# Performance work log

Measured on AMD Instinct MI355X. Metric: run time of the kernel, lower is better.

## Reference

```python
import jax, jax.numpy as jnp
import numpy as np

B, L, S, E = 16, 2048, 2048, 512

def setup_inputs() -> dict:
    key = jax.random.key(0)
    k1, k2, k3 = jax.random.split(key, 3)
    queries = jax.random.normal(k1, (B, L, E), dtype=jnp.float32)
    keys = jax.random.normal(k2, (B, S, E), dtype=jnp.float32)
    values = jax.random.normal(k3, (B, S, E), dtype=jnp.float32)
    # default causal mask: True above the diagonal (positions to mask out)
    attn_mask = jnp.triu(jnp.ones((L, S), dtype=bool), k=1)
    return {"queries": queries, "keys": keys, "values": values, "attn_mask": attn_mask}

def reference(queries, keys, values, attn_mask):
    # queries [B,L,E], keys/values [B,S,E], attn_mask [L,S] bool (True = mask)
    scale = 1.0 / jnp.sqrt(jnp.asarray(queries.shape[-1], queries.dtype))
    scores = jnp.einsum('ble,bse->bls', queries, keys)  # [B,L,S]
    scores = jnp.where(attn_mask, -jnp.inf, scores) * scale
    attn = jax.nn.softmax(scores, axis=-1)  # dropout p=0.0 -> identity
    context = jnp.einsum('bls,bse->ble', attn, values)  # [B,L,E]
    return context
```

## Files before the change

### kernel.cpp

```cpp
#include <hip/hip_runtime.h>

typedef __attribute__((ext_vector_type(4))) float f32x4;
typedef __attribute__((ext_vector_type(16))) float f32x16;
typedef __attribute__((ext_vector_type(8))) short s16x8;
typedef __attribute__((ext_vector_type(8))) unsigned short u16x8;
typedef __attribute__((ext_vector_type(4))) unsigned short u16x4;

#define NB 16
#define SEQ 2048
#define DIM 512
#define QB 64
#define KB 256

__device__ __forceinline__ unsigned short f2bf(float x) {
  unsigned u = __float_as_uint(x);
  u += 0x7fffu + ((u >> 16) & 1u);
  return (unsigned short)(u >> 16);
}

__global__ __launch_bounds__(256) void kf_cvt_kernel(const float* __restrict__ in,
                                                     unsigned short* __restrict__ out) {
  __shared__ float ld[32 * 513];
  const float cs = 0.0637587224f;
  int blk = blockIdx.x;
  int b = blk >> 6, kv32 = blk & 63;
  int t = threadIdx.x;
  const float* src = in + ((size_t)b * SEQ + kv32 * 32) * DIM;
#pragma unroll
  for (int i = 0; i < 16; ++i) {
    int flat = (i * 256 + t) * 4;
    f32x4 a = *(const f32x4*)(src + flat);
    int row = flat >> 9, e = flat & 511;
    float* d = ld + row * 513 + e;
    d[0] = a[0]; d[1] = a[1]; d[2] = a[2]; d[3] = a[3];
  }
  __syncthreads();
  unsigned short* dst = out + (size_t)blk * 16384;
#pragma unroll
  for (int i = 0; i < 8; ++i) {
    int idx8 = i * 256 + t;
    int kstep = idx8 >> 6, ln = idx8 & 63;
    int row = ln & 31, hi = ln >> 5;
    const float* s = ld + row * 513 + kstep * 16 + hi * 8;
    u16x8 o;
#pragma unroll
    for (int j = 0; j < 8; ++j) o[j] = f2bf(s[j] * cs);
    *(u16x8*)(dst + (size_t)idx8 * 8) = o;
  }
}

__global__ __launch_bounds__(256) void vf_cvt_kernel(const float* __restrict__ in,
                                                     unsigned short* __restrict__ out) {
  __shared__ float ld[256 * 33];
  int blk = blockIdx.x;
  int kvc = blk & 7, e32 = (blk >> 3) & 15, b = blk >> 7;
  int t = threadIdx.x;
  const float* src = in + ((size_t)b * SEQ + kvc * 256) * DIM + e32 * 32;
  int r0 = t >> 2, part = t & 3;
#pragma unroll
  for (int i = 0; i < 4; ++i) {
    int row = i * 64 + r0;
    const float* s = src + (size_t)row * DIM + part * 8;
    f32x4 a0 = *(const f32x4*)s;
    f32x4 a1 = *(const f32x4*)(s + 4);
    float* d = ld + row * 33 + part * 8;
    d[0] = a0[0]; d[1] = a0[1]; d[2] = a0[2]; d[3] = a0[3];
    d[4] = a1[0]; d[5] = a1[1]; d[6] = a1[2]; d[7] = a1[3];
  }
  __syncthreads();
  unsigned short* dst = out + (size_t)blk * 8192;
#pragma unroll
  for (int i = 0; i < 4; ++i) {
    int idx8 = i * 256 + t;
    int ksl = idx8 >> 6, ln = idx8 & 63;
    int e = ln & 31, hi = ln >> 5;
    const float* s0 = ld + (ksl * 16 + hi * 8) * 33 + e;
    u16x8 o;
#pragma unroll
    for (int j = 0; j < 8; ++j) o[j] = f2bf(s0[j * 33]);
    *(u16x8*)(dst + (size_t)idx8 * 8) = o;
  }
}

__global__ __launch_bounds__(1024, 1) void attn_kernel(const float* __restrict__ qg,
                                                       const unsigned short* __restrict__ kf,
                                                       const unsigned short* __restrict__ vf,
                                                       float* __restrict__ out) {
  int b = blockIdx.x;
  int y = blockIdx.y;
  int qt = (y < 16) ? y : 47 - y;
  int q0 = qt * QB;

  int tid = threadIdx.x;
  int lane = tid & 63;
  int wid = tid >> 6;
  int l31 = lane & 31;
  int lhi = lane >> 5;
  int mg = wid >> 3, kvq = wid & 7;

  __shared__ unsigned short Qs[2][32][512];
  __shared__ unsigned short Pl[2][64][256];
  __shared__ float cmx[8][68];
  __shared__ float Fs[64];
  __shared__ float Ls[64];

  {
    int q = tid >> 4;
    int ec = (tid & 15) * 32;
    const float* src = qg + ((size_t)b * SEQ + q0 + q) * DIM + ec;
    float v[32];
#pragma unroll
    for (int i = 0; i < 8; ++i) {
      f32x4 a = *(const f32x4*)(src + i * 4);
      v[i * 4 + 0] = a[0]; v[i * 4 + 1] = a[1]; v[i * 4 + 2] = a[2]; v[i * 4 + 3] = a[3];
    }
    int mgq = q >> 5, lq = q & 31;
#pragma unroll
    for (int s = 0; s < 2; ++s) {
      int ks = (ec >> 4) + s;
#pragma unroll
      for (int h = 0; h < 2; ++h) {
        u16x8 o;
#pragma unroll
        for (int j = 0; j < 8; ++j) o[j] = f2bf(v[s * 16 + h * 8 + j]);
        *(u16x8*)&Qs[mgq][ks][(lq + 32 * h) * 8] = o;
      }
    }
  }
  __syncthreads();

  f32x16 oacc[2];
#pragma unroll
  for (int n = 0; n < 2; ++n)
#pragma unroll
    for (int r = 0; r < 16; ++r) oacc[n][r] = 0.f;

  float m_r = -1e30f, l_r = 0.f;
  int qi = mg * 32 + l31;
  unsigned swz = ((unsigned)(qi & 31)) << 4;

  const unsigned short* kfb = kf + ((size_t)b * 64) * 16384;
  int nt = (qt + 4) >> 2;

  for (int t = 0; t < nt; ++t) {
    int pb = t & 1;

    f32x16 sp;
#pragma unroll
    for (int r = 0; r < 16; ++r) sp[r] = 0.f;
    {
      const unsigned short* kp = kfb + ((size_t)(t * 8 + kvq) * 32) * 512 + lane * 8;
#pragma unroll 4
      for (int ks = 0; ks < 32; ++ks) {
        s16x8 a0 = *(const s16x8*)(kp + ks * 512);
        s16x8 b0 = *(const s16x8*)&Qs[mg][ks][lane * 8];
        sp = __builtin_amdgcn_mfma_f32_32x32x16_bf16(a0, b0, sp, 0, 0, 0);
      }
    }

    if (t == nt - 1) {
      int qgl = q0 + qi;
      int kvb = t * 256 + kvq * 32 + 4 * lhi;
#pragma unroll
      for (int r = 0; r < 16; ++r) {
        int kv = kvb + (r & 3) + 8 * (r >> 2);
        if (kv > qgl) sp[r] = -1e30f;
      }
    }

    float cm = sp[0];
#pragma unroll
    for (int r = 1; r < 16; ++r) cm = fmaxf(cm, sp[r]);
    cm = fmaxf(cm, __shfl_xor(cm, 32));
    if (lhi == 0) cmx[kvq][qi] = cm;
    __syncthreads();

    float mt = cmx[0][qi];
#pragma unroll
    for (int c = 1; c < 8; ++c) mt = fmaxf(mt, cmx[c][qi]);
    float m_new = fmaxf(m_r, mt);
    float fsc = exp2f(m_r - m_new);
    m_r = m_new;
    float ps = 0.f;
    u16x4 pk[4];
#pragma unroll
    for (int r = 0; r < 16; ++r) {
      float p = exp2f(sp[r] - m_new);
      ps += p;
      pk[r >> 2][r & 3] = f2bf(p);
    }
    l_r = l_r * fsc + ps;
    {
      char* prow = (char*)&Pl[pb][qi][0];
#pragma unroll
      for (int g = 0; g < 4; ++g) {
        unsigned kvbyte = (unsigned)(kvq * 64 + g * 16 + lhi * 8);
        *(u16x4*)(prow + (kvbyte ^ swz)) = pk[g];
      }
    }
    if (kvq == 0 && lhi == 0) Fs[qi] = fsc;
    __syncthreads();

    {
      f32x4 fr[2][4];
#pragma unroll
      for (int m2 = 0; m2 < 2; ++m2)
#pragma unroll
        for (int g = 0; g < 4; ++g)
          fr[m2][g] = *(const f32x4*)&Fs[m2 * 32 + g * 8 + lhi * 4];
#pragma unroll
      for (int m2 = 0; m2 < 2; ++m2)
#pragma unroll
        for (int r = 0; r < 16; ++r) oacc[m2][r] *= fr[m2][r >> 2][r & 3];

      const unsigned short* vpb =
          vf + (((size_t)b * 16 + wid) * 128 + t * 16) * 512 + lane * 8;
      const char* pr0 = (const char*)&Pl[pb][l31][0];
      const char* pr1 = (const char*)&Pl[pb][32 + l31][0];
      unsigned swzr = ((unsigned)l31) << 4;
#pragma unroll 4
      for (int ks = 0; ks < 16; ++ks) {
        unsigned kb0 = (unsigned)(ks * 32 + lhi * 16);
        s16x8 A0 = *(const s16x8*)(pr0 + (kb0 ^ swzr));
        s16x8 A1 = *(const s16x8*)(pr1 + (kb0 ^ swzr));
        s16x8 B0 = *(const s16x8*)(vpb + ks * 512);
        oacc[0] = __builtin_amdgcn_mfma_f32_32x32x16_bf16(A0, B0, oacc[0], 0, 0, 0);
        oacc[1] = __builtin_amdgcn_mfma_f32_32x32x16_bf16(A1, B0, oacc[1], 0, 0, 0);
      }
    }
  }

  {
    float* lsx = (float*)&Qs[0][0][0];
    __syncthreads();
    lsx[(kvq * 2 + lhi) * 68 + qi] = l_r;
    __syncthreads();
    if (tid < 64) {
      float s = 0.f;
#pragma unroll
      for (int c = 0; c < 16; ++c) s += lsx[c * 68 + tid];
      Ls[tid] = 1.f / s;
    }
    __syncthreads();
  }

  {
    f32x4 li[2][4];
#pragma unroll
    for (int m2 = 0; m2 < 2; ++m2)
#pragma unroll
      for (int g = 0; g < 4; ++g)
        li[m2][g] = *(const f32x4*)&Ls[m2 * 32 + g * 8 + lhi * 4];
#pragma unroll
    for (int m2 = 0; m2 < 2; ++m2)
#pragma unroll
      for (int r = 0; r < 16; ++r) {
        int row = m2 * 32 + (r & 3) + 8 * (r >> 2) + 4 * lhi;
        out[((size_t)b * SEQ + q0 + row) * DIM + wid * 32 + l31] =
            oacc[m2][r] * li[m2][r >> 2][r & 3];
      }
  }
}

extern "C" void kernel_launch(void* const* d_in, const int* in_sizes, int n_in,
                              void* d_out, int out_size, void* d_ws, size_t ws_size,
                              hipStream_t stream) {
  (void)in_sizes; (void)n_in; (void)out_size;
  const float* q = (const float*)d_in[0];
  const float* k = (const float*)d_in[1];
  const float* v = (const float*)d_in[2];
  float* out = (float*)d_out;
  const size_t nelem = (size_t)NB * SEQ * DIM;
  if (ws_size < 2 * nelem * sizeof(unsigned short)) return;
  unsigned short* kfw = (unsigned short*)d_ws;
  unsigned short* vfw = kfw + nelem;

  kf_cvt_kernel<<<NB * 64, 256, 0, stream>>>(k, kfw);
  vf_cvt_kernel<<<NB * 16 * 8, 256, 0, stream>>>(v, vfw);
  dim3 ag(NB, SEQ / QB);
  attn_kernel<<<ag, 1024, 0, stream>>>(q, kfw, vfw, out);
}
```

Measured before the change: 158.4 us.

## Software-pipeline PV of tile t-2 with QK of tile t, one barrier per iteration

Restructures the attention main loop so the P·V MFMAs for tile t-2 are interleaved with the Q·K^T MFMAs for tile t, and the two pending tiles are drained after the loop. The row-max scratch and rescale factors are double-buffered, which removes one __syncthreads per tile and gives the matrix cores two independent accumulation chains to overlap with global loads. The cost is higher register pressure from holding both accumulators and more operand loads inside one loop body. It also adds a separate epilogue code path for the last two tiles.

```diff
diff --git a/kernel.cpp b/kernel.cpp
--- a/kernel.cpp
+++ b/kernel.cpp
@@ -82,6 +82,37 @@
   }
 }
 
+__device__ __forceinline__ void pv_tile_fn(int u, f32x16* oacc,
+                                           const unsigned short* vfb,
+                                           const unsigned short (*Pl)[64][256],
+                                           const float (*Fs)[64], int lane) {
+  int l31 = lane & 31, lhi = lane >> 5;
+  int pb2 = u & 1;
+  const float* fsb = Fs[pb2];
+  f32x4 fr[2][4];
+#pragma unroll
+  for (int m2 = 0; m2 < 2; ++m2)
+#pragma unroll
+    for (int g = 0; g < 4; ++g) fr[m2][g] = *(const f32x4*)&fsb[m2 * 32 + g * 8 + lhi * 4];
+#pragma unroll
+  for (int m2 = 0; m2 < 2; ++m2)
+#pragma unroll
+    for (int r = 0; r < 16; ++r) oacc[m2][r] *= fr[m2][r >> 2][r & 3];
+  const unsigned short* vp = vfb + (size_t)u * 16 * 512 + lane * 8;
+  const char* pr0 = (const char*)&Pl[pb2][l31][0];
+  const char* pr1 = (const char*)&Pl[pb2][32 + l31][0];
+  unsigned swzr = ((unsigned)l31) << 4;
+#pragma unroll 4
+  for (int ks = 0; ks < 16; ++ks) {
+    unsigned kb0 = (unsigned)(ks * 32 + lhi * 16);
+    s16x8 A0 = *(const s16x8*)(pr0 + (kb0 ^ swzr));
+    s16x8 A1 = *(const s16x8*)(pr1 + (kb0 ^ swzr));
+    s16x8 B0 = *(const s16x8*)(vp + ks * 512);
+    oacc[0] = __builtin_amdgcn_mfma_f32_32x32x16_bf16(A0, B0, oacc[0], 0, 0, 0);
+    oacc[1] = __builtin_amdgcn_mfma_f32_32x32x16_bf16(A1, B0, oacc[1], 0, 0, 0);
+  }
+}
+
 __global__ __launch_bounds__(1024, 1) void attn_kernel(const float* __restrict__ qg,
                                                        const unsigned short* __restrict__ kf,
                                                        const unsigned short* __restrict__ vf,
@@ -100,8 +131,8 @@
 
   __shared__ unsigned short Qs[2][32][512];
   __shared__ unsigned short Pl[2][64][256];
-  __shared__ float cmx[8][68];
-  __shared__ float Fs[64];
+  __shared__ float cmx[2][8][68];
+  __shared__ float Fs[2][64];
   __shared__ float Ls[64];
 
   {
@@ -137,20 +168,54 @@
 
   float m_r = -1e30f, l_r = 0.f;
   int qi = mg * 32 + l31;
-  unsigned swz = ((unsigned)(qi & 31)) << 4;
+  unsigned swz = ((unsigned)l31) << 4;
 
   const unsigned short* kfb = kf + ((size_t)b * 64) * 16384;
+  const unsigned short* vfb = vf + ((size_t)b * 16 + wid) * 128 * 512;
   int nt = (qt + 4) >> 2;
 
   for (int t = 0; t < nt; ++t) {
-    int pb = t & 1;
-
     f32x16 sp;
 #pragma unroll
     for (int r = 0; r < 16; ++r) sp[r] = 0.f;
-    {
-      const unsigned short* kp = kfb + ((size_t)(t * 8 + kvq) * 32) * 512 + lane * 8;
+    const unsigned short* kp = kfb + ((size_t)(t * 8 + kvq) * 32) * 512 + lane * 8;
+
+    if (t >= 2) {
+      int u = t - 2, pb2 = u & 1;
+      {
+        const float* fsb = Fs[pb2];
+        f32x4 fr[2][4];
+#pragma unroll
+        for (int m2 = 0; m2 < 2; ++m2)
+#pragma unroll
+          for (int g = 0; g < 4; ++g)
+            fr[m2][g] = *(const f32x4*)&fsb[m2 * 32 + g * 8 + lhi * 4];
+#pragma unroll
+        for (int m2 = 0; m2 < 2; ++m2)
+#pragma unroll
+          for (int r = 0; r < 16; ++r) oacc[m2][r] *= fr[m2][r >> 2][r & 3];
+      }
+      const unsigned short* vp = vfb + (size_t)u * 16 * 512 + lane * 8;
+      const char* pr0 = (const char*)&Pl[pb2][l31][0];
+      const char* pr1 = (const char*)&Pl[pb2][32 + l31][0];
+      unsigned swzr = ((unsigned)l31) << 4;
 #pragma unroll 4
+      for (int j = 0; j < 16; ++j) {
+        s16x8 a0 = *(const s16x8*)(kp + (2 * j) * 512);
+        s16x8 b0 = *(const s16x8*)&Qs[mg][2 * j][lane * 8];
+        s16x8 a1 = *(const s16x8*)(kp + (2 * j + 1) * 512);
+        s16x8 b1 = *(const s16x8*)&Qs[mg][2 * j + 1][lane * 8];
+        unsigned kb0 = (unsigned)(j * 32 + lhi * 16);
+        s16x8 A0 = *(const s16x8*)(pr0 + (kb0 ^ swzr));
+        s16x8 A1 = *(const s16x8*)(pr1 + (kb0 ^ swzr));
+        s16x8 B0 = *(const s16x8*)(vp + j * 512);
+        sp = __builtin_amdgcn_mfma_f32_32x32x16_bf16(a0, b0, sp, 0, 0, 0);
+        oacc[0] = __builtin_amdgcn_mfma_f32_32x32x16_bf16(A0, B0, oacc[0], 0, 0, 0);
+        sp = __builtin_amdgcn_mfma_f32_32x32x16_bf16(a1, b1, sp, 0, 0, 0);
+        oacc[1] = __builtin_amdgcn_mfma_f32_32x32x16_bf16(A1, B0, oacc[1], 0, 0, 0);
+      }
+    } else {
+#pragma unroll 8
       for (int ks = 0; ks < 32; ++ks) {
         s16x8 a0 = *(const s16x8*)(kp + ks * 512);
         s16x8 b0 = *(const s16x8*)&Qs[mg][ks][lane * 8];
@@ -168,71 +233,48 @@
       }
     }
 
-    float cm = sp[0];
-#pragma unroll
-    for (int r = 1; r < 16; ++r) cm = fmaxf(cm, sp[r]);
-    cm = fmaxf(cm, __shfl_xor(cm, 32));
-    if (lhi == 0) cmx[kvq][qi] = cm;
+    {
+      float cm = sp[0];
+#pragma unroll
+      for (int r = 1; r < 16; ++r) cm = fmaxf(cm, sp[r]);
+      cm = fmaxf(cm, __shfl_xor(cm, 32));
+      if (lhi == 0) cmx[t & 1][kvq][qi] = cm;
+    }
     __syncthreads();
 
-    float mt = cmx[0][qi];
-#pragma unroll
-    for (int c = 1; c < 8; ++c) mt = fmaxf(mt, cmx[c][qi]);
-    float m_new = fmaxf(m_r, mt);
-    float fsc = exp2f(m_r - m_new);
-    m_r = m_new;
-    float ps = 0.f;
-    u16x4 pk[4];
-#pragma unroll
-    for (int r = 0; r < 16; ++r) {
-      float p = exp2f(sp[r] - m_new);
-      ps += p;
-      pk[r >> 2][r & 3] = f2bf(p);
-    }
-    l_r = l_r * fsc + ps;
     {
-      char* prow = (char*)&Pl[pb][qi][0];
+      float mt = cmx[t & 1][0][qi];
+#pragma unroll
+      for (int c = 1; c < 8; ++c) mt = fmaxf(mt, cmx[t & 1][c][qi]);
+      float m_new = fmaxf(m_r, mt);
+      float fsc = exp2f(m_r - m_new);
+      m_r = m_new;
+      float ps = 0.f;
+      u16x4 pk[4];
+#pragma unroll
+      for (int r = 0; r < 16; ++r) {
+        float p = exp2f(sp[r] - m_new);
+        ps += p;
+        pk[r >> 2][r & 3] = f2bf(p);
+      }
+      l_r = l_r * fsc + ps;
+      char* prow = (char*)&Pl[t & 1][qi][0];
 #pragma unroll
       for (int g = 0; g < 4; ++g) {
         unsigned kvbyte = (unsigned)(kvq * 64 + g * 16 + lhi * 8);
         *(u16x4*)(prow + (kvbyte ^ swz)) = pk[g];
       }
-    }
-    if (kvq == 0 && lhi == 0) Fs[qi] = fsc;
-    __syncthreads();
-
-    {
-      f32x4 fr[2][4];
-#pragma unroll
-      for (int m2 = 0; m2 < 2; ++m2)
-#pragma unroll
-        for (int g = 0; g < 4; ++g)
-          fr[m2][g] = *(const f32x4*)&Fs[m2 * 32 + g * 8 + lhi * 4];
-#pragma unroll
-      for (int m2 = 0; m2 < 2; ++m2)
-#pragma unroll
-        for (int r = 0; r < 16; ++r) oacc[m2][r] *= fr[m2][r >> 2][r & 3];
-
-      const unsigned short* vpb =
-          vf + (((size_t)b * 16 + wid) * 128 + t * 16) * 512 + lane * 8;
-      const char* pr0 = (const char*)&Pl[pb][l31][0];
-      const char* pr1 = (const char*)&Pl[pb][32 + l31][0];
-      unsigned swzr = ((unsigned)l31) << 4;
-#pragma unroll 4
-      for (int ks = 0; ks < 16; ++ks) {
-        unsigned kb0 = (unsigned)(ks * 32 + lhi * 16);
-        s16x8 A0 = *(const s16x8*)(pr0 + (kb0 ^ swzr));
-        s16x8 A1 = *(const s16x8*)(pr1 + (kb0 ^ swzr));
-        s16x8 B0 = *(const s16x8*)(vpb + ks * 512);
-        oacc[0] = __builtin_amdgcn_mfma_f32_32x32x16_bf16(A0, B0, oacc[0], 0, 0, 0);
-        oacc[1] = __builtin_amdgcn_mfma_f32_32x32x16_bf16(A1, B0, oacc[1], 0, 0, 0);
-      }
-    }
-  }
+      if (kvq == 0 && lhi == 0) Fs[t & 1][qi] = fsc;
+    }
+  }
+
+  if (nt >= 2) pv_tile_fn(nt - 2, oacc, vfb, Pl, Fs, lane);
+  __syncthreads();
+  pv_tile_fn(nt - 1, oacc, vfb, Pl, Fs, lane);
+  __syncthreads();
 
   {
     float* lsx = (float*)&Qs[0][0][0];
-    __syncthreads();
     lsx[(kvq * 2 + lhi) * 68 + qi] = l_r;
     __syncthreads();
     if (tid < 64) {
```

Measured after the change: 155.4 us. About the same (-1.9%).

## Widen KV tile to 512 with each wave covering all 64 query rows

Applied to the files above, without the earlier changes.

Each of the 16 waves now owns a 32-column KV slice and computes scores for both 32-row query halves. This reuses every K fragment for two MFMAs and halves the number of KV iterations and block barriers. Waves whose KV slice lies fully past the causal diagonal skip the QK MFMAs, and the PV loop stops at the last valid KV step. The P buffer is no longer double-buffered. The wider tile can leave more waves idle on the final diagonal tile, and per-thread register pressure rises.

```diff
diff --git a/kernel.cpp b/kernel.cpp
--- a/kernel.cpp
+++ b/kernel.cpp
@@ -10,7 +10,7 @@
 #define SEQ 2048
 #define DIM 512
 #define QB 64
-#define KB 256
+#define KB 512
 
 __device__ __forceinline__ unsigned short f2bf(float x) {
   unsigned u = __float_as_uint(x);
@@ -96,11 +96,11 @@
   int wid = tid >> 6;
   int l31 = lane & 31;
   int lhi = lane >> 5;
-  int mg = wid >> 3, kvq = wid & 7;
+  int kvq = wid;
 
   __shared__ unsigned short Qs[2][32][512];
-  __shared__ unsigned short Pl[2][64][256];
-  __shared__ float cmx[8][68];
+  __shared__ unsigned short Pl[64][512];
+  __shared__ float cmxT[64][20];
   __shared__ float Fs[64];
   __shared__ float Ls[64];
 
@@ -135,70 +135,111 @@
 #pragma unroll
     for (int r = 0; r < 16; ++r) oacc[n][r] = 0.f;
 
-  float m_r = -1e30f, l_r = 0.f;
-  int qi = mg * 32 + l31;
-  unsigned swz = ((unsigned)(qi & 31)) << 4;
+  float m0 = -1e30f, m1 = -1e30f, l0 = 0.f, l1 = 0.f;
+  unsigned swz = ((unsigned)l31) << 5;
 
   const unsigned short* kfb = kf + ((size_t)b * 64) * 16384;
-  int nt = (qt + 4) >> 2;
+  const unsigned short* vfb = vf + ((size_t)b * 16 + wid) * 128 * 512;
+  int nt = (qt + 8) >> 3;
 
   for (int t = 0; t < nt; ++t) {
-    int pb = t & 1;
-
-    f32x16 sp;
-#pragma unroll
-    for (int r = 0; r < 16; ++r) sp[r] = 0.f;
-    {
-      const unsigned short* kp = kfb + ((size_t)(t * 8 + kvq) * 32) * 512 + lane * 8;
+    int kvb = t * 512 + kvq * 32;
+    bool act = kvb <= q0 + 63;
+
+    f32x16 s0, s1;
+    if (act) {
+#pragma unroll
+      for (int r = 0; r < 16; ++r) { s0[r] = 0.f; s1[r] = 0.f; }
+      const unsigned short* kp = kfb + ((size_t)(t * 16 + kvq) * 32) * 512 + lane * 8;
 #pragma unroll 4
       for (int ks = 0; ks < 32; ++ks) {
-        s16x8 a0 = *(const s16x8*)(kp + ks * 512);
-        s16x8 b0 = *(const s16x8*)&Qs[mg][ks][lane * 8];
-        sp = __builtin_amdgcn_mfma_f32_32x32x16_bf16(a0, b0, sp, 0, 0, 0);
-      }
-    }
-
-    if (t == nt - 1) {
-      int qgl = q0 + qi;
-      int kvb = t * 256 + kvq * 32 + 4 * lhi;
+        s16x8 a = *(const s16x8*)(kp + ks * 512);
+        s16x8 b0 = *(const s16x8*)&Qs[0][ks][lane * 8];
+        s16x8 b1 = *(const s16x8*)&Qs[1][ks][lane * 8];
+        s0 = __builtin_amdgcn_mfma_f32_32x32x16_bf16(a, b0, s0, 0, 0, 0);
+        s1 = __builtin_amdgcn_mfma_f32_32x32x16_bf16(a, b1, s1, 0, 0, 0);
+      }
+      if (t == nt - 1) {
+#pragma unroll
+        for (int r = 0; r < 16; ++r) {
+          int kv = kvb + (r & 3) + 8 * (r >> 2) + 4 * lhi;
+          if (kv > q0 + l31) s0[r] = -1e30f;
+          if (kv > q0 + 32 + l31) s1[r] = -1e30f;
+        }
+      }
+    } else {
+#pragma unroll
+      for (int r = 0; r < 16; ++r) { s0[r] = -1e30f; s1[r] = -1e30f; }
+    }
+
+    {
+      float cm0 = s0[0], cm1 = s1[0];
+#pragma unroll
+      for (int r = 1; r < 16; ++r) { cm0 = fmaxf(cm0, s0[r]); cm1 = fmaxf(cm1, s1[r]); }
+      cm0 = fmaxf(cm0, __shfl_xor(cm0, 32));
+      cm1 = fmaxf(cm1, __shfl_xor(cm1, 32));
+      if (lhi == 0) { cmxT[l31][kvq] = cm0; cmxT[32 + l31][kvq] = cm1; }
+    }
+    __syncthreads();
+
+    float fsc0, fsc1;
+    {
+      f32x4 c0 = *(const f32x4*)&cmxT[l31][0];
+      f32x4 c1 = *(const f32x4*)&cmxT[l31][4];
+      f32x4 c2 = *(const f32x4*)&cmxT[l31][8];
+      f32x4 c3 = *(const f32x4*)&cmxT[l31][12];
+      float mt = fmaxf(fmaxf(fmaxf(c0[0], c0[1]), fmaxf(c0[2], c0[3])),
+                       fmaxf(fmaxf(c1[0], c1[1]), fmaxf(c1[2], c1[3])));
+      mt = fmaxf(mt, fmaxf(fmaxf(fmaxf(c2[0], c2[1]), fmaxf(c2[2], c2[3])),
+                           fmaxf(fmaxf(c3[0], c3[1]), fmaxf(c3[2], c3[3]))));
+      float mn = fmaxf(m0, mt);
+      fsc0 = exp2f(m0 - mn);
+      m0 = mn;
+      float ps = 0.f;
+      u16x4 pk[4];
 #pragma unroll
       for (int r = 0; r < 16; ++r) {
-        int kv = kvb + (r & 3) + 8 * (r >> 2);
-        if (kv > qgl) sp[r] = -1e30f;
-      }
-    }
-
-    float cm = sp[0];
-#pragma unroll
-    for (int r = 1; r < 16; ++r) cm = fmaxf(cm, sp[r]);
-    cm = fmaxf(cm, __shfl_xor(cm, 32));
-    if (lhi == 0) cmx[kvq][qi] = cm;
-    __syncthreads();
-
-    float mt = cmx[0][qi];
-#pragma unroll
-    for (int c = 1; c < 8; ++c) mt = fmaxf(mt, cmx[c][qi]);
-    float m_new = fmaxf(m_r, mt);
-    float fsc = exp2f(m_r - m_new);
-    m_r = m_new;
-    float ps = 0.f;
-    u16x4 pk[4];
-#pragma unroll
-    for (int r = 0; r < 16; ++r) {
-      float p = exp2f(sp[r] - m_new);
-      ps += p;
-      pk[r >> 2][r & 3] = f2bf(p);
-    }
-    l_r = l_r * fsc + ps;
-    {
-      char* prow = (char*)&Pl[pb][qi][0];
+        float p = exp2f(s0[r] - mn);
+        ps += p;
+        pk[r >> 2][r & 3] = f2bf(p);
+      }
+      l0 = l0 * fsc0 + ps;
+      char* prow = (char*)&Pl[l31][0];
 #pragma unroll
       for (int g = 0; g < 4; ++g) {
         unsigned kvbyte = (unsigned)(kvq * 64 + g * 16 + lhi * 8);
         *(u16x4*)(prow + (kvbyte ^ swz)) = pk[g];
       }
     }
-    if (kvq == 0 && lhi == 0) Fs[qi] = fsc;
+    {
+      f32x4 c0 = *(const f32x4*)&cmxT[32 + l31][0];
+      f32x4 c1 = *(const f32x4*)&cmxT[32 + l31][4];
+      f32x4 c2 = *(const f32x4*)&cmxT[32 + l31][8];
+      f32x4 c3 = *(const f32x4*)&cmxT[32 + l31][12];
+      float mt = fmaxf(fmaxf(fmaxf(c0[0], c0[1]), fmaxf(c0[2], c0[3])),
+                       fmaxf(fmaxf(c1[0], c1[1]), fmaxf(c1[2], c1[3])));
+      mt = fmaxf(mt, fmaxf(fmaxf(fmaxf(c2[0], c2[1]), fmaxf(c2[2], c2[3])),
+                           fmaxf(fmaxf(c3[0], c3[1]), fmaxf(c3[2], c3[3]))));
+      float mn = fmaxf(m1, mt);
+      fsc1 = exp2f(m1 - mn);
+      m1 = mn;
+      float ps = 0.f;
+      u16x4 pk[4];
+#pragma unroll
+      for (int r = 0; r < 16; ++r) {
+        float p = exp2f(s1[r] - mn);
+        ps += p;
+        pk[r >> 2][r & 3] = f2bf(p);
+      }
+      l1 = l1 * fsc1 + ps;
+      char* prow = (char*)&Pl[32 + l31][0];
+#pragma unroll
+      for (int g = 0; g < 4; ++g) {
+        unsigned kvbyte = (unsigned)(kvq * 64 + g * 16 + lhi * 8);
+        *(u16x4*)(prow + (kvbyte ^ swz)) = pk[g];
+      }
+    }
+    if (wid == 0 && lhi == 0) { Fs[l31] = fsc0; Fs[32 + l31] = fsc1; }
     __syncthreads();
 
     {
@@ -213,17 +254,18 @@
 #pragma unroll
         for (int r = 0; r < 16; ++r) oacc[m2][r] *= fr[m2][r >> 2][r & 3];
 
-      const unsigned short* vpb =
-          vf + (((size_t)b * 16 + wid) * 128 + t * 16) * 512 + lane * 8;
-      const char* pr0 = (const char*)&Pl[pb][l31][0];
-      const char* pr1 = (const char*)&Pl[pb][32 + l31][0];
-      unsigned swzr = ((unsigned)l31) << 4;
+      int kvcnt = q0 + 64 - t * 512;
+      if (kvcnt > 512) kvcnt = 512;
+      int ksb = (kvcnt + 15) >> 4;
+      const unsigned short* vp = vfb + (size_t)(t * 32) * 512 + lane * 8;
+      const char* pr0 = (const char*)&Pl[l31][0];
+      const char* pr1 = (const char*)&Pl[32 + l31][0];
 #pragma unroll 4
-      for (int ks = 0; ks < 16; ++ks) {
+      for (int ks = 0; ks < ksb; ++ks) {
         unsigned kb0 = (unsigned)(ks * 32 + lhi * 16);
-        s16x8 A0 = *(const s16x8*)(pr0 + (kb0 ^ swzr));
-        s16x8 A1 = *(const s16x8*)(pr1 + (kb0 ^ swzr));
-        s16x8 B0 = *(const s16x8*)(vpb + ks * 512);
+        s16x8 A0 = *(const s16x8*)(pr0 + (kb0 ^ swz));
+        s16x8 A1 = *(const s16x8*)(pr1 + (kb0 ^ swz));
+        s16x8 B0 = *(const s16x8*)(vp + ks * 512);
         oacc[0] = __builtin_amdgcn_mfma_f32_32x32x16_bf16(A0, B0, oacc[0], 0, 0, 0);
         oacc[1] = __builtin_amdgcn_mfma_f32_32x32x16_bf16(A1, B0, oacc[1], 0, 0, 0);
       }
@@ -232,13 +274,13 @@
 
   {
     float* lsx = (float*)&Qs[0][0][0];
-    __syncthreads();
-    lsx[(kvq * 2 + lhi) * 68 + qi] = l_r;
+    lsx[(kvq * 2 + lhi) * 68 + l31] = l0;
+    lsx[(kvq * 2 + lhi) * 68 + 32 + l31] = l1;
     __syncthreads();
     if (tid < 64) {
       float s = 0.f;
 #pragma unroll
-      for (int c = 0; c < 16; ++c) s += lsx[c * 68 + tid];
+      for (int c = 0; c < 32; ++c) s += lsx[c * 68 + tid];
       Ls[tid] = 1.f / s;
     }
     __syncthreads();
```

Measured after the change: 154.9 us. -2.2%, faster.

## Double KV tile to 512 with two chunks per wave and causal chunk skipping

Applied to the files above, without the earlier changes.

Each KV tile grows from 256 to 512 keys, so every wave now computes two 32-key score chunks per iteration. This halves the number of outer iterations and block-wide barriers. Chunks lying entirely past the causal diagonal skip their QK MFMAs, and the PV loop is cut to the keys still valid for this query block. The P buffer becomes single-buffered with a narrower swizzle, and the row-max scratch is transposed for vector reads. The trade-off is more live score registers per wave and coarser tiles, which may leave waves idle on short diagonals.

```diff
diff --git a/kernel.cpp b/kernel.cpp
--- a/kernel.cpp
+++ b/kernel.cpp
@@ -10,7 +10,7 @@
 #define SEQ 2048
 #define DIM 512
 #define QB 64
-#define KB 256
+#define KB 512
 
 __device__ __forceinline__ unsigned short f2bf(float x) {
   unsigned u = __float_as_uint(x);
@@ -96,11 +96,12 @@
   int wid = tid >> 6;
   int l31 = lane & 31;
   int lhi = lane >> 5;
-  int mg = wid >> 3, kvq = wid & 7;
+  int qh = wid & 1, dc = wid >> 1;
+  int c0 = dc * 2, c1 = dc * 2 + 1;
 
   __shared__ unsigned short Qs[2][32][512];
-  __shared__ unsigned short Pl[2][64][256];
-  __shared__ float cmx[8][68];
+  __shared__ unsigned short Pl[64][512];
+  __shared__ float cmxT[64][20];
   __shared__ float Fs[64];
   __shared__ float Ls[64];
 
@@ -136,69 +137,98 @@
     for (int r = 0; r < 16; ++r) oacc[n][r] = 0.f;
 
   float m_r = -1e30f, l_r = 0.f;
-  int qi = mg * 32 + l31;
-  unsigned swz = ((unsigned)(qi & 31)) << 4;
+  int qi = qh * 32 + l31;
+  unsigned swz = ((unsigned)(l31 & 7)) << 4;
 
   const unsigned short* kfb = kf + ((size_t)b * 64) * 16384;
-  int nt = (qt + 4) >> 2;
+  const unsigned short* vfb = vf + ((size_t)b * 16 + wid) * 128 * 512;
+  int nt = (qt + 8) >> 3;
 
   for (int t = 0; t < nt; ++t) {
-    int pb = t & 1;
-
-    f32x16 sp;
-#pragma unroll
-    for (int r = 0; r < 16; ++r) sp[r] = 0.f;
+    bool act0 = (t * 512 + c0 * 32) <= q0 + 63;
+    bool act1 = (t * 512 + c1 * 32) <= q0 + 63;
+
+    f32x16 sp0, sp1;
+#pragma unroll
+    for (int r = 0; r < 16; ++r) { sp0[r] = -1e30f; sp1[r] = -1e30f; }
+    if (act0) {
+#pragma unroll
+      for (int r = 0; r < 16; ++r) sp0[r] = 0.f;
+      const unsigned short* kp0 = kfb + ((size_t)(t * 16 + c0) * 32) * 512 + lane * 8;
+      if (act1) {
+#pragma unroll
+        for (int r = 0; r < 16; ++r) sp1[r] = 0.f;
+        const unsigned short* kp1 = kp0 + 32 * 512;
+#pragma unroll
+        for (int ks = 0; ks < 32; ++ks) {
+          s16x8 a0 = *(const s16x8*)(kp0 + ks * 512);
+          s16x8 a1 = *(const s16x8*)(kp1 + ks * 512);
+          s16x8 bq = *(const s16x8*)&Qs[qh][ks][lane * 8];
+          sp0 = __builtin_amdgcn_mfma_f32_32x32x16_bf16(a0, bq, sp0, 0, 0, 0);
+          sp1 = __builtin_amdgcn_mfma_f32_32x32x16_bf16(a1, bq, sp1, 0, 0, 0);
+        }
+      } else {
+#pragma unroll
+        for (int ks = 0; ks < 32; ++ks) {
+          s16x8 a0 = *(const s16x8*)(kp0 + ks * 512);
+          s16x8 bq = *(const s16x8*)&Qs[qh][ks][lane * 8];
+          sp0 = __builtin_amdgcn_mfma_f32_32x32x16_bf16(a0, bq, sp0, 0, 0, 0);
+        }
+      }
+      if (t == nt - 1) {
+        int qgl = q0 + qi;
+#pragma unroll
+        for (int r = 0; r < 16; ++r) {
+          int kvo = (r & 3) + 8 * (r >> 2) + 4 * lhi;
+          if (t * 512 + c0 * 32 + kvo > qgl) sp0[r] = -1e30f;
+          if (t * 512 + c1 * 32 + kvo > qgl) sp1[r] = -1e30f;
+        }
+      }
+    }
+
     {
-      const unsigned short* kp = kfb + ((size_t)(t * 8 + kvq) * 32) * 512 + lane * 8;
-#pragma unroll 4
-      for (int ks = 0; ks < 32; ++ks) {
-        s16x8 a0 = *(const s16x8*)(kp + ks * 512);
-        s16x8 b0 = *(const s16x8*)&Qs[mg][ks][lane * 8];
-        sp = __builtin_amdgcn_mfma_f32_32x32x16_bf16(a0, b0, sp, 0, 0, 0);
-      }
-    }
-
-    if (t == nt - 1) {
-      int qgl = q0 + qi;
-      int kvb = t * 256 + kvq * 32 + 4 * lhi;
+      float cm0 = sp0[0], cm1 = sp1[0];
+#pragma unroll
+      for (int r = 1; r < 16; ++r) { cm0 = fmaxf(cm0, sp0[r]); cm1 = fmaxf(cm1, sp1[r]); }
+      cm0 = fmaxf(cm0, __shfl_xor(cm0, 32));
+      cm1 = fmaxf(cm1, __shfl_xor(cm1, 32));
+      if (lhi == 0) { cmxT[qi][c0] = cm0; cmxT[qi][c1] = cm1; }
+    }
+    __syncthreads();
+
+    {
+      f32x4 cx0 = *(const f32x4*)&cmxT[qi][0];
+      f32x4 cx1 = *(const f32x4*)&cmxT[qi][4];
+      f32x4 cx2 = *(const f32x4*)&cmxT[qi][8];
+      f32x4 cx3 = *(const f32x4*)&cmxT[qi][12];
+      float mt = fmaxf(fmaxf(fmaxf(cx0[0], cx0[1]), fmaxf(cx0[2], cx0[3])),
+                       fmaxf(fmaxf(cx1[0], cx1[1]), fmaxf(cx1[2], cx1[3])));
+      mt = fmaxf(mt, fmaxf(fmaxf(fmaxf(cx2[0], cx2[1]), fmaxf(cx2[2], cx2[3])),
+                           fmaxf(fmaxf(cx3[0], cx3[1]), fmaxf(cx3[2], cx3[3]))));
+      float mn = fmaxf(m_r, mt);
+      float fsc = exp2f(m_r - mn);
+      m_r = mn;
+      float ps = 0.f;
+      u16x4 pk0[4], pk1[4];
 #pragma unroll
       for (int r = 0; r < 16; ++r) {
-        int kv = kvb + (r & 3) + 8 * (r >> 2);
-        if (kv > qgl) sp[r] = -1e30f;
-      }
-    }
-
-    float cm = sp[0];
-#pragma unroll
-    for (int r = 1; r < 16; ++r) cm = fmaxf(cm, sp[r]);
-    cm = fmaxf(cm, __shfl_xor(cm, 32));
-    if (lhi == 0) cmx[kvq][qi] = cm;
-    __syncthreads();
-
-    float mt = cmx[0][qi];
-#pragma unroll
-    for (int c = 1; c < 8; ++c) mt = fmaxf(mt, cmx[c][qi]);
-    float m_new = fmaxf(m_r, mt);
-    float fsc = exp2f(m_r - m_new);
-    m_r = m_new;
-    float ps = 0.f;
-    u16x4 pk[4];
-#pragma unroll
-    for (int r = 0; r < 16; ++r) {
-      float p = exp2f(sp[r] - m_new);
-      ps += p;
-      pk[r >> 2][r & 3] = f2bf(p);
-    }
-    l_r = l_r * fsc + ps;
-    {
-      char* prow = (char*)&Pl[pb][qi][0];
+        float p0 = exp2f(sp0[r] - mn);
+        float p1 = exp2f(sp1[r] - mn);
+        ps += p0 + p1;
+        pk0[r >> 2][r & 3] = f2bf(p0);
+        pk1[r >> 2][r & 3] = f2bf(p1);
+      }
+      l_r = l_r * fsc + ps;
+      char* prow = (char*)&Pl[qi][0];
 #pragma unroll
       for (int g = 0; g < 4; ++g) {
-        unsigned kvbyte = (unsigned)(kvq * 64 + g * 16 + lhi * 8);
-        *(u16x4*)(prow + (kvbyte ^ swz)) = pk[g];
-      }
-    }
-    if (kvq == 0 && lhi == 0) Fs[qi] = fsc;
+        unsigned kb0 = (unsigned)(c0 * 64 + g * 16 + lhi * 8);
+        unsigned kb1 = (unsigned)(c1 * 64 + g * 16 + lhi * 8);
+        *(u16x4*)(prow + (kb0 ^ swz)) = pk0[g];
+        *(u16x4*)(prow + (kb1 ^ swz)) = pk1[g];
+      }
+      if (dc == 0 && lhi == 0) Fs[qi] = fsc;
+    }
     __syncthreads();
 
     {
@@ -213,17 +243,18 @@
 #pragma unroll
         for (int r = 0; r < 16; ++r) oacc[m2][r] *= fr[m2][r >> 2][r & 3];
 
-      const unsigned short* vpb =
-          vf + (((size_t)b * 16 + wid) * 128 + t * 16) * 512 + lane * 8;
-      const char* pr0 = (const char*)&Pl[pb][l31][0];
-      const char* pr1 = (const char*)&Pl[pb][32 + l31][0];
-      unsigned swzr = ((unsigned)l31) << 4;
-#pragma unroll 4
-      for (int ks = 0; ks < 16; ++ks) {
+      int kvcnt = q0 + 64 - t * 512;
+      if (kvcnt > 512) kvcnt = 512;
+      int ksb = (kvcnt + 15) >> 4;
+      const unsigned short* vp = vfb + (size_t)(t * 32) * 512 + lane * 8;
+      const char* pr0 = (const char*)&Pl[l31][0];
+      const char* pr1 = (const char*)&Pl[32 + l31][0];
+#pragma unroll 8
+      for (int ks = 0; ks < ksb; ++ks) {
         unsigned kb0 = (unsigned)(ks * 32 + lhi * 16);
-        s16x8 A0 = *(const s16x8*)(pr0 + (kb0 ^ swzr));
-        s16x8 A1 = *(const s16x8*)(pr1 + (kb0 ^ swzr));
-        s16x8 B0 = *(const s16x8*)(vpb + ks * 512);
+        s16x8 A0 = *(const s16x8*)(pr0 + (kb0 ^ swz));
+        s16x8 A1 = *(const s16x8*)(pr1 + (kb0 ^ swz));
+        s16x8 B0 = *(const s16x8*)(vp + ks * 512);
         oacc[0] = __builtin_amdgcn_mfma_f32_32x32x16_bf16(A0, B0, oacc[0], 0, 0, 0);
         oacc[1] = __builtin_amdgcn_mfma_f32_32x32x16_bf16(A1, B0, oacc[1], 0, 0, 0);
       }
@@ -232,8 +263,7 @@
 
   {
     float* lsx = (float*)&Qs[0][0][0];
-    __syncthreads();
-    lsx[(kvq * 2 + lhi) * 68 + qi] = l_r;
+    lsx[(dc * 2 + lhi) * 68 + qi] = l_r;
     __syncthreads();
     if (tid < 64) {
       float s = 0.f;
```

After: 191.8 us. 21.0% more time.
